# Optimization experiments

Hardware: AMD Instinct MI355X
Metric: run time of the kernel (lower is better)

The kernel has to match this reference:

```python
import jax, jax.numpy as jnp
import numpy as np

TOP_K = 2
NEG_INF = -1.0e9


def setup_inputs() -> dict:
    key = jax.random.key(0)
    k = jax.random.split(key, 5)
    B, S, D, E = 4, 2048, 1024, 8
    H = 2 * D
    x = jax.random.normal(k[0], (B, S, D), dtype=jnp.float32)
    gate_w = jax.random.normal(k[1], (D, E), dtype=jnp.float32) * 0.02
    gate_b = jnp.zeros((E,), dtype=jnp.float32)
    w1 = jax.random.normal(k[2], (E, D, H), dtype=jnp.float32) * 0.02
    b1 = jnp.zeros((E, H), dtype=jnp.float32)
    w2 = jax.random.normal(k[3], (E, H, D), dtype=jnp.float32) * 0.02
    b2 = jnp.zeros((E, D), dtype=jnp.float32)
    noise = jax.random.normal(k[4], (B, S, E), dtype=jnp.float32)
    return {"x": x, "gate_w": gate_w, "gate_b": gate_b,
            "w1": w1, "b1": b1, "w2": w2, "b2": b2, "noise": noise}


def reference(x, gate_w, gate_b, w1, b1, w2, b2, noise):
    B, S, D = x.shape
    # Gating: linear + small gaussian noise (hk.next_rng_key equivalent)
    gating_logits = jnp.einsum('bsd,de->bse', x, gate_w) + gate_b + noise * 0.01
    # keep_top_k: mask all but top-k logits to -1e9
    top_k_values, top_k_indices = jax.lax.top_k(gating_logits, TOP_K)
    mask = gating_logits >= jnp.min(top_k_values, axis=-1, keepdims=True)
    gating_logits = jnp.where(mask, gating_logits, NEG_INF)
    gating_probs = jax.nn.softmax(gating_logits, axis=-1)
    # Dense compute of ALL experts on ALL tokens (as in source): [E,B,S,D]
    h = jax.nn.silu(jnp.einsum('bsd,edh->ebsh', x, w1) + b1[:, None, None, :])
    expert_outputs = jnp.einsum('ebsh,ehd->ebsd', h, w2) + b2[:, None, None, :]
    # Gather top-k expert outputs per token: [B,S,K,D]
    bi = jnp.arange(B)[:, None, None]
    si = jnp.arange(S)[None, :, None]
    selected = expert_outputs[top_k_indices, bi, si]
    top_k_gating_probs = jnp.take_along_axis(gating_probs, top_k_indices, axis=-1)
    final_output = jnp.einsum('bskd,bsk->bsd', selected, top_k_gating_probs)
    # Load-balancing aux loss on the MASKED logits (as in source)
    routing_probs = jax.nn.softmax(gating_logits, axis=-1)
    expert_usage = jnp.sum(routing_probs, axis=(0, 1))
    expert_importance = expert_usage / jnp.sum(expert_usage)
    mean_imp = jnp.mean(expert_importance)
    std_imp = jnp.std(expert_importance)
    aux_loss = std_imp / (mean_imp + 1e-10)
    return final_output, top_k_indices, aux_loss
```

## Files before the change

kernel.cpp:

```cpp
#include <hip/hip_runtime.h>
#include <stdint.h>


#define NTOK   8192
#define DIM    1024
#define NEXP   8
#define HID    2048
#define OUT_MAIN (NTOK * DIM)
#define IDX_OFF  OUT_MAIN
#define AUX_OFF  (OUT_MAIN + NTOK * 2)
#define MAXBLK 72

typedef __attribute__((ext_vector_type(8))) short short8;
typedef __attribute__((ext_vector_type(4))) float floatx4;

__device__ __forceinline__ unsigned short f2bf(float f) {
  unsigned int b = __float_as_uint(f);
  b += 0x7FFFu + ((b >> 16) & 1u);
  return (unsigned short)(b >> 16);
}

__global__ __launch_bounds__(1024) void k_gating(
    const float* __restrict__ x, const float* __restrict__ gate_w,
    const float* __restrict__ gate_b, const float* __restrict__ noise,
    float* __restrict__ out, int* __restrict__ counts,
    int* __restrict__ lists_tok, float* __restrict__ lists_p,
    float* __restrict__ probs_all, unsigned short* __restrict__ xb)
{
  const int lane = threadIdx.x & 63;
  const int wv   = threadIdx.x >> 6;
  const int t    = blockIdx.x * 16 + wv;
  const float* xr = x + (size_t)t * DIM;

  __shared__ int   cnt[NEXP];
  __shared__ int   base[NEXP];
  __shared__ int   s_e[32];
  __shared__ int   s_pos[32];
  __shared__ float s_p[32];
  if (threadIdx.x < NEXP) cnt[threadIdx.x] = 0;

  double acc[NEXP] = {0,0,0,0,0,0,0,0};
  #pragma unroll
  for (int jj = 0; jj < 4; ++jj) {
    const int d0 = lane * 4 + jj * 256;
    const float4 xv = *(const float4*)(xr + d0);
    const float xs[4] = {xv.x, xv.y, xv.z, xv.w};
    unsigned short xbq[4];
    #pragma unroll
    for (int c = 0; c < 4; ++c) {
      const float4 g0 = *(const float4*)(gate_w + (size_t)(d0 + c) * NEXP);
      const float4 g1 = *(const float4*)(gate_w + (size_t)(d0 + c) * NEXP + 4);
      const double xd = (double)xs[c];
      acc[0] += xd * (double)g0.x; acc[1] += xd * (double)g0.y;
      acc[2] += xd * (double)g0.z; acc[3] += xd * (double)g0.w;
      acc[4] += xd * (double)g1.x; acc[5] += xd * (double)g1.y;
      acc[6] += xd * (double)g1.z; acc[7] += xd * (double)g1.w;
      xbq[c] = f2bf(xs[c]);
    }
    ushort4 q; q.x = xbq[0]; q.y = xbq[1]; q.z = xbq[2]; q.w = xbq[3];
    *(ushort4*)(xb + (size_t)t * DIM + d0) = q;
  }
  #pragma unroll
  for (int e = 0; e < NEXP; ++e) {
    #pragma unroll
    for (int off = 32; off; off >>= 1) acc[e] += __shfl_xor(acc[e], off);
  }
  __syncthreads();
  if (lane == 0) {
    double l[NEXP];
    #pragma unroll
    for (int e = 0; e < NEXP; ++e)
      l[e] = acc[e] + (double)gate_b[e] + 0.01 * (double)noise[(size_t)t * NEXP + e];
    int i1 = 0; double v1 = l[0];
    #pragma unroll
    for (int e = 1; e < NEXP; ++e) if (l[e] > v1) { v1 = l[e]; i1 = e; }
    int i2 = (i1 == 0) ? 1 : 0; double v2 = l[i2];
    #pragma unroll
    for (int e = 0; e < NEXP; ++e) if (e != i1 && l[e] > v2) { v2 = l[e]; i2 = e; }
    float pr[NEXP]; float Z = 0.f;
    #pragma unroll
    for (int e = 0; e < NEXP; ++e) {
      const float a = (l[e] >= v2) ? (float)(l[e] - v1) : -1.0e9f;
      pr[e] = __expf(a); Z += pr[e];
    }
    const float rz = 1.0f / Z;
    #pragma unroll
    for (int e = 0; e < NEXP; ++e) {
      pr[e] *= rz;
      probs_all[(size_t)t * NEXP + e] = pr[e];
    }
    out[(size_t)IDX_OFF + t * 2]     = (float)i1;
    out[(size_t)IDX_OFF + t * 2 + 1] = (float)i2;
    const int p1 = atomicAdd(&cnt[i1], 1);
    const int p2 = atomicAdd(&cnt[i2], 1);
    s_e[wv * 2]     = i1; s_pos[wv * 2]     = p1; s_p[wv * 2]     = pr[i1];
    s_e[wv * 2 + 1] = i2; s_pos[wv * 2 + 1] = p2; s_p[wv * 2 + 1] = pr[i2];
  }
  __syncthreads();
  if (threadIdx.x < NEXP) base[threadIdx.x] = atomicAdd(&counts[threadIdx.x], cnt[threadIdx.x]);
  __syncthreads();
  if (lane == 0) {
    #pragma unroll
    for (int k = 0; k < 2; ++k) {
      const int ee  = s_e[wv * 2 + k];
      const int pos = base[ee] + s_pos[wv * 2 + k];
      lists_tok[ee * NTOK + pos] = t;
      lists_p[ee * NTOK + pos]   = s_p[wv * 2 + k];
    }
  }
}

__global__ void k_offs(const int* __restrict__ counts, int* __restrict__ offs,
                       int* __restrict__ tbl_e, int* __restrict__ tbl_m,
                       int* __restrict__ nblk) {
  if (threadIdx.x == 0) {
    int a = 0;
    #pragma unroll
    for (int e = 0; e < NEXP; ++e) { offs[e] = a; a += counts[e]; }
    offs[NEXP] = a;
    int ent_e[MAXBLK], ent_m[MAXBLK];
    int nb = 0;
    for (int e = 0; e < NEXP; ++e) {
      const int nbe = (counts[e] + 255) >> 8;
      for (int m = 0; m < nbe; ++m) { ent_e[nb] = e; ent_m[nb] = m << 8; ++nb; }
    }
    nblk[0] = nb;
    for (int p = 0; p < MAXBLK; ++p) { tbl_e[p] = -1; tbl_m[p] = 0; }
    const int q = nb >> 3, r = nb & 7;
    for (int c = 0; c < 8; ++c) {
      const int cnt   = q + (c < r ? 1 : 0);
      const int start = c * q + (c < r ? c : r);
      for (int t = 0; t < cnt; ++t) {
        const int pos = c + (t << 3);
        tbl_e[pos] = ent_e[start + t];
        tbl_m[pos] = ent_m[start + t];
      }
    }
  }
}

__global__ __launch_bounds__(256) void k_aux(const float* __restrict__ probs_all,
                                             float* __restrict__ out) {
  float p[NEXP] = {0,0,0,0,0,0,0,0};
  for (int t = threadIdx.x; t < NTOK; t += 256) {
    const float4 a = *(const float4*)(probs_all + (size_t)t * NEXP);
    const float4 b = *(const float4*)(probs_all + (size_t)t * NEXP + 4);
    p[0] += a.x; p[1] += a.y; p[2] += a.z; p[3] += a.w;
    p[4] += b.x; p[5] += b.y; p[6] += b.z; p[7] += b.w;
  }
  #pragma unroll
  for (int e = 0; e < NEXP; ++e) {
    #pragma unroll
    for (int off = 32; off; off >>= 1) p[e] += __shfl_xor(p[e], off);
  }
  __shared__ float red[4][NEXP];
  const int lane = threadIdx.x & 63, wv = threadIdx.x >> 6;
  if (lane == 0) {
    #pragma unroll
    for (int e = 0; e < NEXP; ++e) red[wv][e] = p[e];
  }
  __syncthreads();
  if (threadIdx.x == 0) {
    float usage[NEXP], s = 0.f;
    #pragma unroll
    for (int e = 0; e < NEXP; ++e) {
      usage[e] = red[0][e] + red[1][e] + red[2][e] + red[3][e];
      s += usage[e];
    }
    float imp[NEXP], mean = 0.f, var = 0.f;
    #pragma unroll
    for (int e = 0; e < NEXP; ++e) { imp[e] = usage[e] / s; mean += imp[e]; }
    mean *= 0.125f;
    #pragma unroll
    for (int e = 0; e < NEXP; ++e) { const float d = imp[e] - mean; var += d * d; }
    var *= 0.125f;
    out[AUX_OFF] = sqrtf(var) / (mean + 1e-10f);
  }
}

__global__ __launch_bounds__(256) void k_tr(
    const float* __restrict__ in, unsigned short* __restrict__ out,
    int in_ld, size_t in_estride, int r0, int c0,
    int out_ld, size_t out_estride)
{
  const int e  = blockIdx.z;
  const int tr = blockIdx.x << 6;
  const int tc = blockIdx.y << 6;
  const int tid = threadIdx.x;
  __shared__ float t[64][65];
  const float* src = in + (size_t)e * in_estride + (size_t)(r0 + tr) * in_ld + (c0 + tc);
  #pragma unroll
  for (int p = 0; p < 4; ++p) {
    const int r  = (p << 4) + (tid >> 4);
    const int c4 = (tid & 15) << 2;
    const float4 v = *(const float4*)(src + (size_t)r * in_ld + c4);
    t[r][c4] = v.x; t[r][c4 + 1] = v.y; t[r][c4 + 2] = v.z; t[r][c4 + 3] = v.w;
  }
  __syncthreads();
  unsigned short* dst = out + (size_t)e * out_estride + (size_t)tc * out_ld + tr;
  #pragma unroll
  for (int p = 0; p < 4; ++p) {
    const int c  = (p << 4) + (tid >> 4);
    const int r4 = (tid & 15) << 2;
    ushort4 q;
    q.x = f2bf(t[r4][c]);     q.y = f2bf(t[r4 + 1][c]);
    q.z = f2bf(t[r4 + 2][c]); q.w = f2bf(t[r4 + 3][c]);
    *(ushort4*)(dst + (size_t)c * out_ld + r4) = q;
  }
}

template <int MODE>
__global__ __launch_bounds__(1024) void k_gemm(
    const unsigned short* __restrict__ Abase,
    const unsigned short* __restrict__ Bt,
    const float* __restrict__ bias,
    const int* __restrict__ counts, const int* __restrict__ offs,
    const int* __restrict__ tbl_e, const int* __restrict__ tbl_m,
    const int* __restrict__ nblk,
    const int* __restrict__ lists_tok, const float* __restrict__ lists_p,
    unsigned short* __restrict__ hout, float* __restrict__ out,
    const int hb, const int Hs)
{
  const int bx = blockIdx.x;
  const int e  = tbl_e[bx];
  if (e < 0) return;
  const int m0  = tbl_m[bx];
  const int n_e = counts[e];
  const int by  = blockIdx.y;

  int nb, k0g, Kloc;
  if (MODE == 0) { nb = by << 8; k0g = 0; Kloc = DIM; }
  else { nb = (by >> 1) << 8; const int half = Hs >> 1;
         k0g = (by & 1) * half; Kloc = half; }

  const int tid  = threadIdx.x;
  const int lane = tid & 63;
  const int wv   = tid >> 6;
  const int wm   = (wv & 3) << 6;
  const int wn   = (wv >> 2) << 6;

  __shared__ __align__(16) unsigned short as[2][256 * 64];
  __shared__ __align__(16) unsigned short bs[2][256 * 64];

  const int K = (MODE == 0) ? DIM : Hs;
  const unsigned short* Bexp = Bt + (size_t)e * ((size_t)DIM * Hs) + (size_t)nb * K + k0g;

  const int off_sh = ((lane & 7) ^ (lane >> 3)) << 3;
  const int Ra0 = wv * 8 + (lane >> 3);
  const int Ra1 = 128 + Ra0;
  const int rc0 = (m0 + Ra0 < n_e) ? (m0 + Ra0) : (n_e - 1);
  const int rc1 = (m0 + Ra1 < n_e) ? (m0 + Ra1) : (n_e - 1);
  size_t arow0, arow1;
  if (MODE == 0) {
    arow0 = (size_t)lists_tok[e * NTOK + rc0] * DIM;
    arow1 = (size_t)lists_tok[e * NTOK + rc1] * DIM;
  } else {
    arow0 = (size_t)(offs[e] + rc0) * Hs;
    arow1 = (size_t)(offs[e] + rc1) * Hs;
  }
  const unsigned short* gpa0 = Abase + arow0 + k0g + off_sh;
  const unsigned short* gpa1 = Abase + arow1 + k0g + off_sh;
  const unsigned short* gpb0 = Bexp + (size_t)Ra0 * K + off_sh;
  const unsigned short* gpb1 = Bexp + (size_t)Ra1 * K + off_sh;

  floatx4 acc[4][4];
  #pragma unroll
  for (int i = 0; i < 4; ++i)
    #pragma unroll
    for (int j2 = 0; j2 < 4; ++j2) acc[i][j2] = (floatx4){0.f, 0.f, 0.f, 0.f};

  auto issue = [&](int buf, int kk) {
    unsigned short* a0 = (buf ? &as[1][0] : &as[0][0]) + wv * 8 * 64;
    unsigned short* b0 = (buf ? &bs[1][0] : &bs[0][0]) + wv * 8 * 64;
    __builtin_amdgcn_global_load_lds(
        (const __attribute__((address_space(1))) void*)(gpa0 + kk),
        (__attribute__((address_space(3))) void*)(void*)a0, 16, 0, 0);
    __builtin_amdgcn_global_load_lds(
        (const __attribute__((address_space(1))) void*)(gpa1 + kk),
        (__attribute__((address_space(3))) void*)(void*)(a0 + 128 * 64), 16, 0, 0);
    __builtin_amdgcn_global_load_lds(
        (const __attribute__((address_space(1))) void*)(gpb0 + kk),
        (__attribute__((address_space(3))) void*)(void*)b0, 16, 0, 0);
    __builtin_amdgcn_global_load_lds(
        (const __attribute__((address_space(1))) void*)(gpb1 + kk),
        (__attribute__((address_space(3))) void*)(void*)(b0 + 128 * 64), 16, 0, 0);
  };

  const int nt = Kloc >> 6;
  issue(0, 0);
  issue(1, 64);
  int p = 0;
  for (int t = 0; t < nt; ++t) {
    if (t + 1 < nt) { asm volatile("s_waitcnt vmcnt(4)" ::: "memory"); }
    else            { asm volatile("s_waitcnt vmcnt(0)" ::: "memory"); }
    __builtin_amdgcn_sched_barrier(0);
    __builtin_amdgcn_s_barrier();
    __builtin_amdgcn_sched_barrier(0);
    const unsigned short* ap = p ? &as[1][0] : &as[0][0];
    const unsigned short* bp = p ? &bs[1][0] : &bs[0][0];
    const int c = lane >> 4;
    #pragma unroll
    for (int s = 0; s < 2; ++s) {
      short8 af[4], bfr[4];
      #pragma unroll
      for (int i = 0; i < 4; ++i) {
        const int row = wm + (i << 4) + (lane & 15);
        af[i] = *(const short8*)(ap + row * 64 + ((((s << 2) | c) ^ (row & 7)) << 3));
      }
      #pragma unroll
      for (int j2 = 0; j2 < 4; ++j2) {
        const int row = wn + (j2 << 4) + (lane & 15);
        bfr[j2] = *(const short8*)(bp + row * 64 + ((((s << 2) | c) ^ (row & 7)) << 3));
      }
      __builtin_amdgcn_s_setprio(1);
      #pragma unroll
      for (int i = 0; i < 4; ++i)
        #pragma unroll
        for (int j2 = 0; j2 < 4; ++j2)
          acc[i][j2] = __builtin_amdgcn_mfma_f32_16x16x32_bf16(af[i], bfr[j2], acc[i][j2], 0, 0, 0);
      __builtin_amdgcn_s_setprio(0);
    }
    __builtin_amdgcn_sched_barrier(0);
    __builtin_amdgcn_s_barrier();
    __builtin_amdgcn_sched_barrier(0);
    if (t + 2 < nt) issue(p, (t + 2) << 6);
    p ^= 1;
  }

  const int q4 = (lane >> 4) << 2;
  if (MODE == 0) {
    #pragma unroll
    for (int i = 0; i < 4; ++i) {
      #pragma unroll
      for (int j2 = 0; j2 < 4; ++j2) {
        const int nloc = wn + (j2 << 4) + (lane & 15);
        const float bb = bias[e * HID + hb + nb + nloc];
        #pragma unroll
        for (int rr = 0; rr < 4; ++rr) {
          const int m = m0 + wm + (i << 4) + q4 + rr;
          if (m < n_e) {
            float v = acc[i][j2][rr] + bb;
            v = v / (1.0f + __expf(-v));
            hout[(size_t)(offs[e] + m) * Hs + nb + nloc] = f2bf(v);
          }
        }
      }
    }
  } else {
    #pragma unroll
    for (int i = 0; i < 4; ++i) {
      #pragma unroll
      for (int rr = 0; rr < 4; ++rr) {
        const int m = m0 + wm + (i << 4) + q4 + rr;
        if (m < n_e) {
          const int   tok = lists_tok[e * NTOK + m];
          const float pp  = lists_p[e * NTOK + m];
          #pragma unroll
          for (int j2 = 0; j2 < 4; ++j2) {
            const int d = nb + wn + (j2 << 4) + (lane & 15);
            float v = acc[i][j2][rr];
            if (hb == 0 && k0g == 0) v += bias[e * DIM + d];
            atomicAdd(out + (size_t)tok * DIM + d, pp * v);
          }
        }
      }
    }
  }
}

extern "C" void kernel_launch(void* const* d_in, const int* in_sizes, int n_in,
                              void* d_out, int out_size, void* d_ws, size_t ws_size,
                              hipStream_t stream)
{
  const float* x      = (const float*)d_in[0];
  const float* gate_w = (const float*)d_in[1];
  const float* gate_b = (const float*)d_in[2];
  const float* w1     = (const float*)d_in[3];
  const float* b1     = (const float*)d_in[4];
  const float* w2     = (const float*)d_in[5];
  const float* b2     = (const float*)d_in[6];
  const float* noise  = (const float*)d_in[7];
  float* out = (float*)d_out;

  char* ws = (char*)d_ws;
  const size_t CNT_OFF = 0;
  const size_t OFF_OFF = 64;
  const size_t NBK_OFF = 128;
  const size_t TBE_OFF = 192;
  const size_t TBM_OFF = 1024;
  const size_t LT_OFF  = 2048;
  const size_t LP_OFF  = LT_OFF + 262144;
  const size_t PA_OFF  = LP_OFF + 262144;
  const size_t XB_OFF  = 1048576;
  const size_t W_OFF   = 17825792;

  int nsl = 0;
  for (int cand = 1; cand <= 8; cand <<= 1) {
    const size_t need = W_OFF + (size_t)(33554432 + 67108864) / (size_t)cand;
    if (ws_size >= need) { nsl = cand; break; }
  }
  if (!nsl) return;
  const int Hs = HID / nsl;

  int* counts          = (int*)(ws + CNT_OFF);
  int* offs            = (int*)(ws + OFF_OFF);
  int* nblk            = (int*)(ws + NBK_OFF);
  int* tbl_e           = (int*)(ws + TBE_OFF);
  int* tbl_m           = (int*)(ws + TBM_OFF);
  int* lists_tok       = (int*)(ws + LT_OFF);
  float* lists_p       = (float*)(ws + LP_OFF);
  float* probs_all     = (float*)(ws + PA_OFF);
  unsigned short* xb   = (unsigned short*)(ws + XB_OFF);
  unsigned short* wt   = (unsigned short*)(ws + W_OFF);
  unsigned short* hbuf = (unsigned short*)(ws + W_OFF + (size_t)33554432 / nsl);

  hipMemsetAsync(d_out, 0, (size_t)OUT_MAIN * sizeof(float), stream);
  hipMemsetAsync(ws + CNT_OFF, 0, 64, stream);

  k_gating<<<NTOK / 16, 1024, 0, stream>>>(x, gate_w, gate_b, noise, out, counts,
                                           lists_tok, lists_p, probs_all, xb);
  k_offs<<<1, 64, 0, stream>>>(counts, offs, tbl_e, tbl_m, nblk);
  k_aux<<<1, 256, 0, stream>>>(probs_all, out);

  for (int s = 0; s < nsl; ++s) {
    const int hb = s * Hs;
    dim3 gt1(DIM / 64, Hs / 64, NEXP);
    k_tr<<<gt1, 256, 0, stream>>>(w1, wt, HID, (size_t)DIM * HID, 0, hb,
                                  DIM, (size_t)Hs * DIM);
    dim3 g1(MAXBLK, Hs / 256, 1);
    k_gemm<0><<<g1, 1024, 0, stream>>>(xb, wt, b1, counts, offs, tbl_e, tbl_m, nblk,
                                       lists_tok, lists_p, hbuf, out, hb, Hs);
    dim3 gt2(Hs / 64, DIM / 64, NEXP);
    k_tr<<<gt2, 256, 0, stream>>>(w2, wt, DIM, (size_t)DIM * HID, hb, 0,
                                  Hs, (size_t)DIM * Hs);
    dim3 g2(MAXBLK, (DIM / 256) * 2, 1);
    k_gemm<1><<<g2, 1024, 0, stream>>>(hbuf, wt, b2, counts, offs, tbl_e, tbl_m, nblk,
                                       lists_tok, lists_p, hbuf, out, hb, Hs);
  }
}
```

Baseline: 409.0 us.

## Restructure expert GEMM to 8 waves with 128x64 warp tiles and interleaved staging

The grouped expert GEMM moves from 16 waves per block to 8 waves, each owning a 128x64 output tile, with launch bounds allowing two blocks per CU. The K loop is split into four sub-phases, and each global-to-LDS stage for the next tile is interleaved with LDS fragment loads and MFMA bursts. The second GEMM no longer splits K into two halves, which halves the atomic adds to the output but also halves the grid parallelism. The change is meant to raise MFMA density and fragment reuse, at the cost of higher register pressure and more barriers per iteration.

```diff
diff --git a/kernel.cpp b/kernel.cpp
--- a/kernel.cpp
+++ b/kernel.cpp
@@ -210,7 +210,7 @@
 }
 
 template <int MODE>
-__global__ __launch_bounds__(1024) void k_gemm(
+__global__ __launch_bounds__(512, 2) void k_gemm(
     const unsigned short* __restrict__ Abase,
     const unsigned short* __restrict__ Bt,
     const float* __restrict__ bias,
@@ -226,120 +226,196 @@
   if (e < 0) return;
   const int m0  = tbl_m[bx];
   const int n_e = counts[e];
-  const int by  = blockIdx.y;
-
-  int nb, k0g, Kloc;
-  if (MODE == 0) { nb = by << 8; k0g = 0; Kloc = DIM; }
-  else { nb = (by >> 1) << 8; const int half = Hs >> 1;
-         k0g = (by & 1) * half; Kloc = half; }
+  const int nb  = blockIdx.y << 8;
+
+  const int Kloc = (MODE == 0) ? DIM : Hs;
+  const int nt   = Kloc >> 6;
 
   const int tid  = threadIdx.x;
   const int lane = tid & 63;
   const int wv   = tid >> 6;
-  const int wm   = (wv & 3) << 6;
-  const int wn   = (wv >> 2) << 6;
+  const int wm   = (wv & 1) << 7;
+  const int wn   = (wv >> 1) << 6;
 
   __shared__ __align__(16) unsigned short as[2][256 * 64];
   __shared__ __align__(16) unsigned short bs[2][256 * 64];
-
-  const int K = (MODE == 0) ? DIM : Hs;
-  const unsigned short* Bexp = Bt + (size_t)e * ((size_t)DIM * Hs) + (size_t)nb * K + k0g;
+  unsigned short* const A0 = &as[0][0]; unsigned short* const A1 = &as[1][0];
+  unsigned short* const B0 = &bs[0][0]; unsigned short* const B1 = &bs[1][0];
+
+  const unsigned short* Bexp = Bt + (size_t)e * ((size_t)DIM * Hs) + (size_t)nb * Kloc;
 
   const int off_sh = ((lane & 7) ^ (lane >> 3)) << 3;
-  const int Ra0 = wv * 8 + (lane >> 3);
-  const int Ra1 = 128 + Ra0;
-  const int rc0 = (m0 + Ra0 < n_e) ? (m0 + Ra0) : (n_e - 1);
-  const int rc1 = (m0 + Ra1 < n_e) ? (m0 + Ra1) : (n_e - 1);
-  size_t arow0, arow1;
-  if (MODE == 0) {
-    arow0 = (size_t)lists_tok[e * NTOK + rc0] * DIM;
-    arow1 = (size_t)lists_tok[e * NTOK + rc1] * DIM;
-  } else {
-    arow0 = (size_t)(offs[e] + rc0) * Hs;
-    arow1 = (size_t)(offs[e] + rc1) * Hs;
-  }
-  const unsigned short* gpa0 = Abase + arow0 + k0g + off_sh;
-  const unsigned short* gpa1 = Abase + arow1 + k0g + off_sh;
-  const unsigned short* gpb0 = Bexp + (size_t)Ra0 * K + off_sh;
-  const unsigned short* gpb1 = Bexp + (size_t)Ra1 * K + off_sh;
-
-  floatx4 acc[4][4];
+  const int r0  = (wv << 3) + (lane >> 3);
+  const int rb0 = ((wv >> 2) << 6) + ((wv & 3) << 3) + (lane >> 3);
+  const unsigned short* pA0; const unsigned short* pA1;
+  const unsigned short* pA2; const unsigned short* pA3;
+  {
+    const unsigned short* p[4];
+    #pragma unroll
+    for (int qq = 0; qq < 4; ++qq) {
+      const int rr = m0 + r0 + (qq << 6);
+      const int rc = (rr < n_e) ? rr : (n_e - 1);
+      size_t arow;
+      if (MODE == 0) arow = (size_t)lists_tok[e * NTOK + rc] * DIM;
+      else           arow = (size_t)(offs[e] + rc) * Hs;
+      p[qq] = Abase + arow + off_sh;
+    }
+    pA0 = p[0]; pA1 = p[1]; pA2 = p[2]; pA3 = p[3];
+  }
+  const unsigned short* pB0 = Bexp + (size_t)rb0 * Kloc + off_sh;
+  const unsigned short* pB1 = Bexp + (size_t)(rb0 + 32) * Kloc + off_sh;
+  const unsigned short* pB2 = Bexp + (size_t)(rb0 + 128) * Kloc + off_sh;
+  const unsigned short* pB3 = Bexp + (size_t)(rb0 + 160) * Kloc + off_sh;
+  const int dA = (wv << 3) * 64;
+  const int dB = (((wv >> 2) << 6) + ((wv & 3) << 3)) * 64;
+
+  auto ST = [&](const unsigned short* g, unsigned short* l) {
+    __builtin_amdgcn_global_load_lds(
+        (const __attribute__((address_space(1))) void*)g,
+        (__attribute__((address_space(3))) void*)(void*)l, 16, 0, 0);
+  };
+  auto STG_A0 = [&](unsigned short* ab, int t) { if (t < nt) { const int kk = t << 6;
+      ST(pA0 + kk, ab + dA); ST(pA2 + kk, ab + 2 * 4096 + dA); } };
+  auto STG_A1 = [&](unsigned short* ab, int t) { if (t < nt) { const int kk = t << 6;
+      ST(pA1 + kk, ab + 4096 + dA); ST(pA3 + kk, ab + 3 * 4096 + dA); } };
+  auto STG_B0 = [&](unsigned short* bb, int t) { if (t < nt) { const int kk = t << 6;
+      ST(pB0 + kk, bb + dB); ST(pB2 + kk, bb + 8192 + dB); } };
+  auto STG_B1 = [&](unsigned short* bb, int t) { if (t < nt) { const int kk = t << 6;
+      ST(pB1 + kk, bb + 2048 + dB); ST(pB3 + kk, bb + 10240 + dB); } };
+
+  auto LDA8 = [&](const unsigned short* ab, int i, int s) -> short8 {
+    const int row = wm + (i << 4) + (lane & 15);
+    const int ck  = (((s << 2) | (lane >> 4)) ^ (row & 7)) << 3;
+    return *(const short8*)(ab + row * 64 + ck);
+  };
+  auto LDB8 = [&](const unsigned short* bb, int j, int s) -> short8 {
+    const int row = wn + (j << 4) + (lane & 15);
+    const int ck  = (((s << 2) | (lane >> 4)) ^ (row & 7)) << 3;
+    return *(const short8*)(bb + row * 64 + ck);
+  };
+
+  floatx4 acc[8][4];
   #pragma unroll
-  for (int i = 0; i < 4; ++i)
-    #pragma unroll
-    for (int j2 = 0; j2 < 4; ++j2) acc[i][j2] = (floatx4){0.f, 0.f, 0.f, 0.f};
-
-  auto issue = [&](int buf, int kk) {
-    unsigned short* a0 = (buf ? &as[1][0] : &as[0][0]) + wv * 8 * 64;
-    unsigned short* b0 = (buf ? &bs[1][0] : &bs[0][0]) + wv * 8 * 64;
-    __builtin_amdgcn_global_load_lds(
-        (const __attribute__((address_space(1))) void*)(gpa0 + kk),
-        (__attribute__((address_space(3))) void*)(void*)a0, 16, 0, 0);
-    __builtin_amdgcn_global_load_lds(
-        (const __attribute__((address_space(1))) void*)(gpa1 + kk),
-        (__attribute__((address_space(3))) void*)(void*)(a0 + 128 * 64), 16, 0, 0);
-    __builtin_amdgcn_global_load_lds(
-        (const __attribute__((address_space(1))) void*)(gpb0 + kk),
-        (__attribute__((address_space(3))) void*)(void*)b0, 16, 0, 0);
-    __builtin_amdgcn_global_load_lds(
-        (const __attribute__((address_space(1))) void*)(gpb1 + kk),
-        (__attribute__((address_space(3))) void*)(void*)(b0 + 128 * 64), 16, 0, 0);
-  };
-
-  const int nt = Kloc >> 6;
-  issue(0, 0);
-  issue(1, 64);
-  int p = 0;
-  for (int t = 0; t < nt; ++t) {
-    if (t + 1 < nt) { asm volatile("s_waitcnt vmcnt(4)" ::: "memory"); }
+  for (int i = 0; i < 8; ++i)
+    #pragma unroll
+    for (int j = 0; j < 4; ++j) acc[i][j] = (floatx4){0.f, 0.f, 0.f, 0.f};
+
+  STG_A0(A0, 0); STG_B1(B0, 0); STG_A1(A0, 0); STG_B0(B0, 0);
+  STG_A0(A1, 1); STG_B1(B1, 1); STG_A1(A1, 1);
+
+  short8 a_[4][2], b_[2][2];
+  for (int u = 0; u < nt; ++u) {
+    const int p = u & 1;
+    const unsigned short* ap = p ? A1 : A0;
+    const unsigned short* bp = p ? B1 : B0;
+    unsigned short* apn = p ? A0 : A1;
+    unsigned short* apc = p ? A1 : A0;
+    unsigned short* bpn = p ? B0 : B1;
+    unsigned short* bpc = p ? B1 : B0;
+    (void)apn;
+
+    STG_B0(bpn, u + 1);
+    if (u + 1 < nt) { asm volatile("s_waitcnt vmcnt(8)" ::: "memory"); }
     else            { asm volatile("s_waitcnt vmcnt(0)" ::: "memory"); }
     __builtin_amdgcn_sched_barrier(0);
     __builtin_amdgcn_s_barrier();
     __builtin_amdgcn_sched_barrier(0);
-    const unsigned short* ap = p ? &as[1][0] : &as[0][0];
-    const unsigned short* bp = p ? &bs[1][0] : &bs[0][0];
-    const int c = lane >> 4;
-    #pragma unroll
-    for (int s = 0; s < 2; ++s) {
-      short8 af[4], bfr[4];
-      #pragma unroll
-      for (int i = 0; i < 4; ++i) {
-        const int row = wm + (i << 4) + (lane & 15);
-        af[i] = *(const short8*)(ap + row * 64 + ((((s << 2) | c) ^ (row & 7)) << 3));
-      }
-      #pragma unroll
-      for (int j2 = 0; j2 < 4; ++j2) {
-        const int row = wn + (j2 << 4) + (lane & 15);
-        bfr[j2] = *(const short8*)(bp + row * 64 + ((((s << 2) | c) ^ (row & 7)) << 3));
-      }
-      __builtin_amdgcn_s_setprio(1);
+    #pragma unroll
+    for (int i = 0; i < 4; ++i) { a_[i][0] = LDA8(ap, i, 0); a_[i][1] = LDA8(ap, i, 1); }
+    #pragma unroll
+    for (int j = 0; j < 2; ++j) { b_[j][0] = LDB8(bp, j, 0); b_[j][1] = LDB8(bp, j, 1); }
+    asm volatile("s_waitcnt lgkmcnt(0)" ::: "memory");
+    __builtin_amdgcn_sched_barrier(0);
+    __builtin_amdgcn_s_setprio(1);
+    #pragma unroll
+    for (int s = 0; s < 2; ++s)
       #pragma unroll
       for (int i = 0; i < 4; ++i)
         #pragma unroll
-        for (int j2 = 0; j2 < 4; ++j2)
-          acc[i][j2] = __builtin_amdgcn_mfma_f32_16x16x32_bf16(af[i], bfr[j2], acc[i][j2], 0, 0, 0);
-      __builtin_amdgcn_s_setprio(0);
-    }
-    __builtin_amdgcn_sched_barrier(0);
-    __builtin_amdgcn_s_barrier();
-    __builtin_amdgcn_sched_barrier(0);
-    if (t + 2 < nt) issue(p, (t + 2) << 6);
-    p ^= 1;
+        for (int j = 0; j < 2; ++j)
+          acc[i][j] = __builtin_amdgcn_mfma_f32_16x16x32_bf16(a_[i][s], b_[j][s], acc[i][j], 0, 0, 0);
+    __builtin_amdgcn_s_setprio(0);
+    __builtin_amdgcn_sched_barrier(0);
+    __builtin_amdgcn_s_barrier();
+    __builtin_amdgcn_sched_barrier(0);
+
+    STG_A0(apc, u + 2);
+    #pragma unroll
+    for (int j = 0; j < 2; ++j) { b_[j][0] = LDB8(bp, j + 2, 0); b_[j][1] = LDB8(bp, j + 2, 1); }
+    __builtin_amdgcn_sched_barrier(0);
+    __builtin_amdgcn_s_barrier();
+    __builtin_amdgcn_sched_barrier(0);
+    asm volatile("s_waitcnt lgkmcnt(0)" ::: "memory");
+    __builtin_amdgcn_sched_barrier(0);
+    __builtin_amdgcn_s_setprio(1);
+    #pragma unroll
+    for (int s = 0; s < 2; ++s)
+      #pragma unroll
+      for (int i = 0; i < 4; ++i)
+        #pragma unroll
+        for (int j = 0; j < 2; ++j)
+          acc[i][j + 2] = __builtin_amdgcn_mfma_f32_16x16x32_bf16(a_[i][s], b_[j][s], acc[i][j + 2], 0, 0, 0);
+    __builtin_amdgcn_s_setprio(0);
+    __builtin_amdgcn_sched_barrier(0);
+    __builtin_amdgcn_s_barrier();
+    __builtin_amdgcn_sched_barrier(0);
+
+    STG_B1(bpc, u + 2);
+    #pragma unroll
+    for (int i = 0; i < 4; ++i) { a_[i][0] = LDA8(ap, i + 4, 0); a_[i][1] = LDA8(ap, i + 4, 1); }
+    __builtin_amdgcn_sched_barrier(0);
+    __builtin_amdgcn_s_barrier();
+    __builtin_amdgcn_sched_barrier(0);
+    asm volatile("s_waitcnt lgkmcnt(0)" ::: "memory");
+    __builtin_amdgcn_sched_barrier(0);
+    __builtin_amdgcn_s_setprio(1);
+    #pragma unroll
+    for (int s = 0; s < 2; ++s)
+      #pragma unroll
+      for (int i = 0; i < 4; ++i)
+        #pragma unroll
+        for (int j = 0; j < 2; ++j)
+          acc[i + 4][j + 2] = __builtin_amdgcn_mfma_f32_16x16x32_bf16(a_[i][s], b_[j][s], acc[i + 4][j + 2], 0, 0, 0);
+    __builtin_amdgcn_s_setprio(0);
+    __builtin_amdgcn_sched_barrier(0);
+    __builtin_amdgcn_s_barrier();
+    __builtin_amdgcn_sched_barrier(0);
+
+    STG_A1(apc, u + 2);
+    #pragma unroll
+    for (int j = 0; j < 2; ++j) { b_[j][0] = LDB8(bp, j, 0); b_[j][1] = LDB8(bp, j, 1); }
+    __builtin_amdgcn_sched_barrier(0);
+    __builtin_amdgcn_s_barrier();
+    __builtin_amdgcn_sched_barrier(0);
+    asm volatile("s_waitcnt lgkmcnt(0)" ::: "memory");
+    __builtin_amdgcn_sched_barrier(0);
+    __builtin_amdgcn_s_setprio(1);
+    #pragma unroll
+    for (int s = 0; s < 2; ++s)
+      #pragma unroll
+      for (int i = 0; i < 4; ++i)
+        #pragma unroll
+        for (int j = 0; j < 2; ++j)
+          acc[i + 4][j] = __builtin_amdgcn_mfma_f32_16x16x32_bf16(a_[i][s], b_[j][s], acc[i + 4][j], 0, 0, 0);
+    __builtin_amdgcn_s_setprio(0);
+    __builtin_amdgcn_sched_barrier(0);
+    __builtin_amdgcn_s_barrier();
+    __builtin_amdgcn_sched_barrier(0);
   }
 
   const int q4 = (lane >> 4) << 2;
   if (MODE == 0) {
     #pragma unroll
-    for (int i = 0; i < 4; ++i) {
+    for (int i = 0; i < 8; ++i) {
       #pragma unroll
-      for (int j2 = 0; j2 < 4; ++j2) {
-        const int nloc = wn + (j2 << 4) + (lane & 15);
+      for (int j = 0; j < 4; ++j) {
+        const int nloc = wn + (j << 4) + (lane & 15);
         const float bb = bias[e * HID + hb + nb + nloc];
         #pragma unroll
         for (int rr = 0; rr < 4; ++rr) {
           const int m = m0 + wm + (i << 4) + q4 + rr;
           if (m < n_e) {
-            float v = acc[i][j2][rr] + bb;
+            float v = acc[i][j][rr] + bb;
             v = v / (1.0f + __expf(-v));
             hout[(size_t)(offs[e] + m) * Hs + nb + nloc] = f2bf(v);
           }
@@ -348,7 +424,7 @@
     }
   } else {
     #pragma unroll
-    for (int i = 0; i < 4; ++i) {
+    for (int i = 0; i < 8; ++i) {
       #pragma unroll
       for (int rr = 0; rr < 4; ++rr) {
         const int m = m0 + wm + (i << 4) + q4 + rr;
@@ -356,10 +432,10 @@
           const int   tok = lists_tok[e * NTOK + m];
           const float pp  = lists_p[e * NTOK + m];
           #pragma unroll
-          for (int j2 = 0; j2 < 4; ++j2) {
-            const int d = nb + wn + (j2 << 4) + (lane & 15);
-            float v = acc[i][j2][rr];
-            if (hb == 0 && k0g == 0) v += bias[e * DIM + d];
+          for (int j = 0; j < 4; ++j) {
+            const int d = nb + wn + (j << 4) + (lane & 15);
+            float v = acc[i][j][rr];
+            if (hb == 0) v += bias[e * DIM + d];
             atomicAdd(out + (size_t)tok * DIM + d, pp * v);
           }
         }
@@ -428,13 +504,13 @@
     k_tr<<<gt1, 256, 0, stream>>>(w1, wt, HID, (size_t)DIM * HID, 0, hb,
                                   DIM, (size_t)Hs * DIM);
     dim3 g1(MAXBLK, Hs / 256, 1);
-    k_gemm<0><<<g1, 1024, 0, stream>>>(xb, wt, b1, counts, offs, tbl_e, tbl_m, nblk,
-                                       lists_tok, lists_p, hbuf, out, hb, Hs);
+    k_gemm<0><<<g1, 512, 0, stream>>>(xb, wt, b1, counts, offs, tbl_e, tbl_m, nblk,
+                                      lists_tok, lists_p, hbuf, out, hb, Hs);
     dim3 gt2(Hs / 64, DIM / 64, NEXP);
     k_tr<<<gt2, 256, 0, stream>>>(w2, wt, DIM, (size_t)DIM * HID, hb, 0,
                                   Hs, (size_t)DIM * Hs);
-    dim3 g2(MAXBLK, (DIM / 256) * 2, 1);
-    k_gemm<1><<<g2, 1024, 0, stream>>>(hbuf, wt, b2, counts, offs, tbl_e, tbl_m, nblk,
-                                       lists_tok, lists_p, hbuf, out, hb, Hs);
-  }
-}
+    dim3 g2(MAXBLK, DIM / 256, 1);
+    k_gemm<1><<<g2, 512, 0, stream>>>(hbuf, wt, b2, counts, offs, tbl_e, tbl_m, nblk,
+                                      lists_tok, lists_p, hbuf, out, hb, Hs);
+  }
+}
```

Result: slower. 496.4 us (+21.4%).

## Shrink grouped GEMM tiles to 128x128x32 with 256-thread blocks

Applied to the files above, without the earlier changes.

Changes the expert GEMM tiling from 256x256 tiles with a K-step of 64 and 1024 threads to 128x128 tiles with a K-step of 32 and 256 threads. MAXBLK, the block tables and the LDS swizzle are updated to match, and launch bounds now allow 4 blocks per CU. The goal is more blocks in flight, better occupancy and less padding waste on partial expert tiles, at the cost of less data reuse per tile and more barriers. It also merges the offsets and aux-loss kernels into one launch.

```diff
diff --git a/kernel.cpp b/kernel.cpp
--- a/kernel.cpp
+++ b/kernel.cpp
@@ -9,7 +9,7 @@
 #define OUT_MAIN (NTOK * DIM)
 #define IDX_OFF  OUT_MAIN
 #define AUX_OFF  (OUT_MAIN + NTOK * 2)
-#define MAXBLK 72
+#define MAXBLK 144
 
 typedef __attribute__((ext_vector_type(8))) short short8;
 typedef __attribute__((ext_vector_type(4))) float floatx4;
@@ -110,9 +110,11 @@
   }
 }
 
-__global__ void k_offs(const int* __restrict__ counts, int* __restrict__ offs,
-                       int* __restrict__ tbl_e, int* __restrict__ tbl_m,
-                       int* __restrict__ nblk) {
+__global__ __launch_bounds__(256) void k_meta(
+    const int* __restrict__ counts, int* __restrict__ offs,
+    int* __restrict__ tbl_e, int* __restrict__ tbl_m, int* __restrict__ nblk,
+    const float* __restrict__ probs_all, float* __restrict__ out)
+{
   if (threadIdx.x == 0) {
     int a = 0;
     #pragma unroll
@@ -121,26 +123,22 @@
     int ent_e[MAXBLK], ent_m[MAXBLK];
     int nb = 0;
     for (int e = 0; e < NEXP; ++e) {
-      const int nbe = (counts[e] + 255) >> 8;
-      for (int m = 0; m < nbe; ++m) { ent_e[nb] = e; ent_m[nb] = m << 8; ++nb; }
+      const int nbe = (counts[e] + 127) >> 7;
+      for (int m = 0; m < nbe; ++m) { ent_e[nb] = e; ent_m[nb] = m << 7; ++nb; }
     }
     nblk[0] = nb;
     for (int p = 0; p < MAXBLK; ++p) { tbl_e[p] = -1; tbl_m[p] = 0; }
     const int q = nb >> 3, r = nb & 7;
     for (int c = 0; c < 8; ++c) {
-      const int cnt   = q + (c < r ? 1 : 0);
+      const int cc    = q + (c < r ? 1 : 0);
       const int start = c * q + (c < r ? c : r);
-      for (int t = 0; t < cnt; ++t) {
+      for (int t = 0; t < cc; ++t) {
         const int pos = c + (t << 3);
         tbl_e[pos] = ent_e[start + t];
         tbl_m[pos] = ent_m[start + t];
       }
     }
   }
-}
-
-__global__ __launch_bounds__(256) void k_aux(const float* __restrict__ probs_all,
-                                             float* __restrict__ out) {
   float p[NEXP] = {0,0,0,0,0,0,0,0};
   for (int t = threadIdx.x; t < NTOK; t += 256) {
     const float4 a = *(const float4*)(probs_all + (size_t)t * NEXP);
@@ -210,7 +208,7 @@
 }
 
 template <int MODE>
-__global__ __launch_bounds__(1024) void k_gemm(
+__global__ __launch_bounds__(256, 4) void k_gemm(
     const unsigned short* __restrict__ Abase,
     const unsigned short* __restrict__ Bt,
     const float* __restrict__ bias,
@@ -229,27 +227,28 @@
   const int by  = blockIdx.y;
 
   int nb, k0g, Kloc;
-  if (MODE == 0) { nb = by << 8; k0g = 0; Kloc = DIM; }
-  else { nb = (by >> 1) << 8; const int half = Hs >> 1;
+  if (MODE == 0) { nb = by << 7; k0g = 0; Kloc = DIM; }
+  else { nb = (by >> 1) << 7; const int half = Hs >> 1;
          k0g = (by & 1) * half; Kloc = half; }
 
   const int tid  = threadIdx.x;
   const int lane = tid & 63;
   const int wv   = tid >> 6;
-  const int wm   = (wv & 3) << 6;
-  const int wn   = (wv >> 2) << 6;
-
-  __shared__ __align__(16) unsigned short as[2][256 * 64];
-  __shared__ __align__(16) unsigned short bs[2][256 * 64];
+  const int wm   = (wv & 1) << 6;
+  const int wn   = (wv >> 1) << 6;
+
+  __shared__ __align__(16) unsigned short as[2][128 * 32];
+  __shared__ __align__(16) unsigned short bs[2][128 * 32];
 
   const int K = (MODE == 0) ? DIM : Hs;
   const unsigned short* Bexp = Bt + (size_t)e * ((size_t)DIM * Hs) + (size_t)nb * K + k0g;
 
-  const int off_sh = ((lane & 7) ^ (lane >> 3)) << 3;
-  const int Ra0 = wv * 8 + (lane >> 3);
-  const int Ra1 = 128 + Ra0;
-  const int rc0 = (m0 + Ra0 < n_e) ? (m0 + Ra0) : (n_e - 1);
-  const int rc1 = (m0 + Ra1 < n_e) ? (m0 + Ra1) : (n_e - 1);
+  const int off_sh = (((lane & 3) ^ ((lane >> 3) & 3)) << 3);
+  const int rA = (wv << 5) + (lane >> 2);
+  const int rr0 = m0 + rA;
+  const int rr1 = m0 + rA + 16;
+  const int rc0 = (rr0 < n_e) ? rr0 : (n_e - 1);
+  const int rc1 = (rr1 < n_e) ? rr1 : (n_e - 1);
   size_t arow0, arow1;
   if (MODE == 0) {
     arow0 = (size_t)lists_tok[e * NTOK + rc0] * DIM;
@@ -260,35 +259,36 @@
   }
   const unsigned short* gpa0 = Abase + arow0 + k0g + off_sh;
   const unsigned short* gpa1 = Abase + arow1 + k0g + off_sh;
-  const unsigned short* gpb0 = Bexp + (size_t)Ra0 * K + off_sh;
-  const unsigned short* gpb1 = Bexp + (size_t)Ra1 * K + off_sh;
-
-  floatx4 acc[4][4];
-  #pragma unroll
-  for (int i = 0; i < 4; ++i)
-    #pragma unroll
-    for (int j2 = 0; j2 < 4; ++j2) acc[i][j2] = (floatx4){0.f, 0.f, 0.f, 0.f};
+  const unsigned short* gpb0 = Bexp + (size_t)rA * K + off_sh;
+  const unsigned short* gpb1 = Bexp + (size_t)(rA + 16) * K + off_sh;
+  const int dbase = (wv << 5) * 32;
 
   auto issue = [&](int buf, int kk) {
-    unsigned short* a0 = (buf ? &as[1][0] : &as[0][0]) + wv * 8 * 64;
-    unsigned short* b0 = (buf ? &bs[1][0] : &bs[0][0]) + wv * 8 * 64;
+    unsigned short* a0 = (buf ? &as[1][0] : &as[0][0]) + dbase;
+    unsigned short* b0 = (buf ? &bs[1][0] : &bs[0][0]) + dbase;
     __builtin_amdgcn_global_load_lds(
         (const __attribute__((address_space(1))) void*)(gpa0 + kk),
         (__attribute__((address_space(3))) void*)(void*)a0, 16, 0, 0);
     __builtin_amdgcn_global_load_lds(
         (const __attribute__((address_space(1))) void*)(gpa1 + kk),
-        (__attribute__((address_space(3))) void*)(void*)(a0 + 128 * 64), 16, 0, 0);
+        (__attribute__((address_space(3))) void*)(void*)(a0 + 16 * 32), 16, 0, 0);
     __builtin_amdgcn_global_load_lds(
         (const __attribute__((address_space(1))) void*)(gpb0 + kk),
         (__attribute__((address_space(3))) void*)(void*)b0, 16, 0, 0);
     __builtin_amdgcn_global_load_lds(
         (const __attribute__((address_space(1))) void*)(gpb1 + kk),
-        (__attribute__((address_space(3))) void*)(void*)(b0 + 128 * 64), 16, 0, 0);
+        (__attribute__((address_space(3))) void*)(void*)(b0 + 16 * 32), 16, 0, 0);
   };
 
-  const int nt = Kloc >> 6;
+  floatx4 acc[4][4];
+  #pragma unroll
+  for (int i = 0; i < 4; ++i)
+    #pragma unroll
+    for (int j2 = 0; j2 < 4; ++j2) acc[i][j2] = (floatx4){0.f, 0.f, 0.f, 0.f};
+
+  const int nt = Kloc >> 5;
   issue(0, 0);
-  issue(1, 64);
+  issue(1, 32);
   int p = 0;
   for (int t = 0; t < nt; ++t) {
     if (t + 1 < nt) { asm volatile("s_waitcnt vmcnt(4)" ::: "memory"); }
@@ -299,31 +299,28 @@
     const unsigned short* ap = p ? &as[1][0] : &as[0][0];
     const unsigned short* bp = p ? &bs[1][0] : &bs[0][0];
     const int c = lane >> 4;
-    #pragma unroll
-    for (int s = 0; s < 2; ++s) {
-      short8 af[4], bfr[4];
+    short8 af[4], bfr[4];
+    #pragma unroll
+    for (int i = 0; i < 4; ++i) {
+      const int row = wm + (i << 4) + (lane & 15);
+      af[i] = *(const short8*)(ap + (row << 5) + ((c ^ ((row >> 1) & 3)) << 3));
+    }
+    #pragma unroll
+    for (int j2 = 0; j2 < 4; ++j2) {
+      const int row = wn + (j2 << 4) + (lane & 15);
+      bfr[j2] = *(const short8*)(bp + (row << 5) + ((c ^ ((row >> 1) & 3)) << 3));
+    }
+    __builtin_amdgcn_s_setprio(1);
+    #pragma unroll
+    for (int i = 0; i < 4; ++i)
       #pragma unroll
-      for (int i = 0; i < 4; ++i) {
-        const int row = wm + (i << 4) + (lane & 15);
-        af[i] = *(const short8*)(ap + row * 64 + ((((s << 2) | c) ^ (row & 7)) << 3));
-      }
-      #pragma unroll
-      for (int j2 = 0; j2 < 4; ++j2) {
-        const int row = wn + (j2 << 4) + (lane & 15);
-        bfr[j2] = *(const short8*)(bp + row * 64 + ((((s << 2) | c) ^ (row & 7)) << 3));
-      }
-      __builtin_amdgcn_s_setprio(1);
-      #pragma unroll
-      for (int i = 0; i < 4; ++i)
-        #pragma unroll
-        for (int j2 = 0; j2 < 4; ++j2)
-          acc[i][j2] = __builtin_amdgcn_mfma_f32_16x16x32_bf16(af[i], bfr[j2], acc[i][j2], 0, 0, 0);
-      __builtin_amdgcn_s_setprio(0);
-    }
+      for (int j2 = 0; j2 < 4; ++j2)
+        acc[i][j2] = __builtin_amdgcn_mfma_f32_16x16x32_bf16(af[i], bfr[j2], acc[i][j2], 0, 0, 0);
+    __builtin_amdgcn_s_setprio(0);
     __builtin_amdgcn_sched_barrier(0);
     __builtin_amdgcn_s_barrier();
     __builtin_amdgcn_sched_barrier(0);
-    if (t + 2 < nt) issue(p, (t + 2) << 6);
+    if (t + 2 < nt) issue(p, (t + 2) << 5);
     p ^= 1;
   }
 
@@ -388,7 +385,7 @@
   const size_t NBK_OFF = 128;
   const size_t TBE_OFF = 192;
   const size_t TBM_OFF = 1024;
-  const size_t LT_OFF  = 2048;
+  const size_t LT_OFF  = 4096;
   const size_t LP_OFF  = LT_OFF + 262144;
   const size_t PA_OFF  = LP_OFF + 262144;
   const size_t XB_OFF  = 1048576;
@@ -419,22 +416,21 @@
 
   k_gating<<<NTOK / 16, 1024, 0, stream>>>(x, gate_w, gate_b, noise, out, counts,
                                            lists_tok, lists_p, probs_all, xb);
-  k_offs<<<1, 64, 0, stream>>>(counts, offs, tbl_e, tbl_m, nblk);
-  k_aux<<<1, 256, 0, stream>>>(probs_all, out);
+  k_meta<<<1, 256, 0, stream>>>(counts, offs, tbl_e, tbl_m, nblk, probs_all, out);
 
   for (int s = 0; s < nsl; ++s) {
     const int hb = s * Hs;
     dim3 gt1(DIM / 64, Hs / 64, NEXP);
     k_tr<<<gt1, 256, 0, stream>>>(w1, wt, HID, (size_t)DIM * HID, 0, hb,
                                   DIM, (size_t)Hs * DIM);
-    dim3 g1(MAXBLK, Hs / 256, 1);
-    k_gemm<0><<<g1, 1024, 0, stream>>>(xb, wt, b1, counts, offs, tbl_e, tbl_m, nblk,
-                                       lists_tok, lists_p, hbuf, out, hb, Hs);
+    dim3 g1(MAXBLK, Hs / 128, 1);
+    k_gemm<0><<<g1, 256, 0, stream>>>(xb, wt, b1, counts, offs, tbl_e, tbl_m, nblk,
+                                      lists_tok, lists_p, hbuf, out, hb, Hs);
     dim3 gt2(Hs / 64, DIM / 64, NEXP);
     k_tr<<<gt2, 256, 0, stream>>>(w2, wt, DIM, (size_t)DIM * HID, hb, 0,
                                   Hs, (size_t)DIM * Hs);
-    dim3 g2(MAXBLK, (DIM / 256) * 2, 1);
-    k_gemm<1><<<g2, 1024, 0, stream>>>(hbuf, wt, b2, counts, offs, tbl_e, tbl_m, nblk,
-                                       lists_tok, lists_p, hbuf, out, hb, Hs);
-  }
-}
+    dim3 g2(MAXBLK, (DIM / 128) * 2, 1);
+    k_gemm<1><<<g2, 256, 0, stream>>>(hbuf, wt, b2, counts, offs, tbl_e, tbl_m, nblk,
+                                      lists_tok, lists_p, hbuf, out, hb, Hs);
+  }
+}
```

New measurement: 424.8 us. +3.8%, slower.
